# Kernel tuning notes

Hardware: AMD Instinct MI355X
Metric: run time of the kernel (lower is better)

## Reference

```python
import jax, jax.numpy as jnp
import numpy as np

B, L, D, C = 4, 512, 128, 128
EPS = 1e-7  # Keras backend epsilon


def setup_inputs() -> dict:
    key = jax.random.key(0)
    ks = jax.random.split(key, 4)
    inps = jax.random.normal(ks[0], (B, L, D), dtype=jnp.float32)
    # glorot_normal-ish scale for weights
    wei_t = jax.random.normal(ks[1], (D, C), dtype=jnp.float32) * (2.0 / (D + C)) ** 0.5
    wei_x = jax.random.normal(ks[2], (D, C), dtype=jnp.float32) * (2.0 / (D + C)) ** 0.5
    bxh = jnp.zeros((C,), dtype=jnp.float32)
    wei_a = jax.random.normal(ks[3], (C,), dtype=jnp.float32) * (2.0 / (C + 1)) ** 0.5
    bxa = jnp.zeros((), dtype=jnp.float32)
    return {"inps": inps, "wei_t": wei_t, "wei_x": wei_x, "bxh": bxh,
            "wei_a": wei_a, "bxa": bxa}


def reference(inps, wei_t, wei_x, bxh, wei_a, bxa):
    # Additive (Bahdanau-style) pairwise self-attention, no mask.
    qt = inps @ wei_t                      # [B, L, C] (query-side projection)
    kx = inps @ wei_x                      # [B, L, C] (key-side projection)
    # Pairwise hidden: [B, L, L, C]
    h = jnp.tanh(qt[:, :, None, :] + kx[:, None, :, :] + bxh)
    scores = jnp.einsum('bijc,c->bij', h, wei_a) + bxa  # [B, L, L]
    # activation_func=None -> linear (identity)
    e = jnp.exp(scores - jnp.max(scores, axis=-1, keepdims=True))
    a = e / (jnp.sum(e, axis=-1, keepdims=True) + EPS)   # [B, L, L]
    out = jnp.einsum('bij,bjd->bid', a, inps)            # [B, L, D]
    return out
```

## Files before the change

### kernel.cpp

```cpp
#include <hip/hip_runtime.h>

#define NB 4
#define SL 512
#define DD 128
#define CC 128

__device__ __forceinline__ float fexp2(float x) { return __builtin_amdgcn_exp2f(x); }
__device__ __forceinline__ float frcp(float x)  { return __builtin_amdgcn_rcpf(x); }

__global__ __launch_bounds__(256) void proj_kernel(
    const float* __restrict__ inps, const float* __restrict__ wei_t,
    const float* __restrict__ wei_x, const float* __restrict__ bxh,
    float* __restrict__ E, float* __restrict__ F)
{
    const float K2 = 2.8853900817779268f;
    const int row0 = blockIdx.x * 2;
    const int b    = row0 >> 9;
    const int i0   = row0 & 511;
    const int c    = threadIdx.x & 127;
    const int sel  = threadIdx.x >> 7;

    const float* W  = sel ? wei_x : wei_t;
    const float* r0 = inps + (size_t)row0 * DD;
    const float* r1 = r0 + DD;

    float a0 = 0.f, a1 = 0.f;
    #pragma unroll 8
    for (int k = 0; k < DD; ++k) {
        float w = W[k * CC + c];
        a0 = fmaf(r0[k], w, a0);
        a1 = fmaf(r1[k], w, a1);
    }

    if (sel == 0) {
        float bb = bxh[c];
        E[(size_t)(row0 + 0) * CC + c] = fexp2(K2 * (a0 + bb));
        E[(size_t)(row0 + 1) * CC + c] = fexp2(K2 * (a1 + bb));
    } else {
        float2 v = {fexp2(K2 * a0), fexp2(K2 * a1)};
        *reinterpret_cast<float2*>(&F[((size_t)b * CC + c) * SL + i0]) = v;
    }
}

__global__ __launch_bounds__(1024, 8) void attn_kernel(
    const float* __restrict__ inps, const float* __restrict__ wei_a,
    const float* __restrict__ E, const float* __restrict__ F,
    float* __restrict__ out)
{
    __shared__ float4 upk[CC];
    __shared__ float pool[4 * 16 * DD];
    __shared__ float scT[SL * 4];
    __shared__ float redw[4 * 4];

    const int blk = blockIdx.x;
    const int b   = blk >> 7;
    const int i0  = (blk & 127) * 4;
    const int bi0 = b * SL + i0;
    const int tid = threadIdx.x;
    const int jt  = tid & 255;
    const int cq  = tid >> 8;
    const int j0  = jt * 2;

    if (tid < CC) {
        float4 u;
        u.x = E[(size_t)(bi0 + 0) * CC + tid];
        u.y = E[(size_t)(bi0 + 1) * CC + tid];
        u.z = E[(size_t)(bi0 + 2) * CC + tid];
        u.w = E[(size_t)(bi0 + 3) * CC + tid];
        upk[tid] = u;
    }
    __syncthreads();

    const int c0 = cq * 32;
    const float* fb = F + ((size_t)b * CC + c0) * SL + j0;
    const float4* up = upk + c0;
    const float* wa = wei_a + c0;
    float sx[4] = {0.f, 0.f, 0.f, 0.f};
    float sy[4] = {0.f, 0.f, 0.f, 0.f};
    #pragma unroll 4
    for (int cp = 0; cp < 16; ++cp) {
        float2 f0 = *reinterpret_cast<const float2*>(&fb[(size_t)(2 * cp) * SL]);
        float2 f1 = *reinterpret_cast<const float2*>(&fb[(size_t)(2 * cp + 1) * SL]);
        float4 u0 = up[2 * cp];
        float4 u1 = up[2 * cp + 1];
        float wa0 = wa[2 * cp], wa1 = wa[2 * cp + 1];
        const float* u0p = reinterpret_cast<const float*>(&u0);
        const float* u1p = reinterpret_cast<const float*>(&u1);
        #pragma unroll
        for (int i = 0; i < 4; ++i) {
            float ax = fmaf(u0p[i], f0.x, 1.0f);
            float bx = fmaf(u1p[i], f1.x, 1.0f);
            float numx = fmaf(wa0, bx, wa1 * ax);
            sx[i] = fmaf(numx, frcp(ax * bx), sx[i]);
            float ay = fmaf(u0p[i], f0.y, 1.0f);
            float by = fmaf(u1p[i], f1.y, 1.0f);
            float numy = fmaf(wa0, by, wa1 * ay);
            sy[i] = fmaf(numy, frcp(ay * by), sy[i]);
        }
    }

    if (cq > 0) {
        float* m = &pool[(cq - 1) * 2304 + jt * 9];
        #pragma unroll
        for (int i = 0; i < 4; ++i) { m[i] = sx[i]; m[4 + i] = sy[i]; }
    }
    __syncthreads();

    if (cq == 0) {
        #pragma unroll
        for (int seg = 0; seg < 3; ++seg) {
            const float* m = &pool[seg * 2304 + jt * 9];
            #pragma unroll
            for (int i = 0; i < 4; ++i) { sx[i] += m[i]; sy[i] += m[4 + i]; }
        }
        const float KE = -2.8853900817779268f;
        float ex[4], ey[4];
        const int lane = tid & 63, wv = tid >> 6;
        #pragma unroll
        for (int i = 0; i < 4; ++i) {
            ex[i] = fexp2(sx[i] * KE);
            ey[i] = fexp2(sy[i] * KE);
            float t = ex[i] + ey[i];
            #pragma unroll
            for (int off = 32; off > 0; off >>= 1)
                t += __shfl_xor(t, off, 64);
            if (lane == 0) redw[i * 4 + wv] = t;
        }
        __syncthreads();
        float4 av0, av1;
        {
            float S0 = redw[0] + redw[1] + redw[2] + redw[3];
            float S1 = redw[4] + redw[5] + redw[6] + redw[7];
            float S2 = redw[8] + redw[9] + redw[10] + redw[11];
            float S3 = redw[12] + redw[13] + redw[14] + redw[15];
            float r0 = frcp(S0 + 1e-7f), r1 = frcp(S1 + 1e-7f);
            float r2 = frcp(S2 + 1e-7f), r3 = frcp(S3 + 1e-7f);
            av0 = make_float4(ex[0] * r0, ex[1] * r1, ex[2] * r2, ex[3] * r3);
            av1 = make_float4(ey[0] * r0, ey[1] * r1, ey[2] * r2, ey[3] * r3);
        }
        *reinterpret_cast<float4*>(&scT[j0 * 4])     = av0;
        *reinterpret_cast<float4*>(&scT[j0 * 4 + 4]) = av1;
    } else {
        __syncthreads();
    }
    __syncthreads();

    if (tid < 512) {
        const int dq = (tid & 31) * 4;
        const int jq = tid >> 5;
        const float* ibase = inps + (size_t)b * SL * DD;
        float4 acc0 = {0,0,0,0}, acc1 = {0,0,0,0}, acc2 = {0,0,0,0}, acc3 = {0,0,0,0};
        const int jb = jq * 32;
        #pragma unroll 4
        for (int jj = 0; jj < 32; ++jj) {
            int jx = jb + jj;
            float4 v  = *reinterpret_cast<const float4*>(ibase + (size_t)jx * DD + dq);
            float4 a4 = *reinterpret_cast<const float4*>(&scT[jx * 4]);
            acc0.x = fmaf(a4.x, v.x, acc0.x); acc0.y = fmaf(a4.x, v.y, acc0.y);
            acc0.z = fmaf(a4.x, v.z, acc0.z); acc0.w = fmaf(a4.x, v.w, acc0.w);
            acc1.x = fmaf(a4.y, v.x, acc1.x); acc1.y = fmaf(a4.y, v.y, acc1.y);
            acc1.z = fmaf(a4.y, v.z, acc1.z); acc1.w = fmaf(a4.y, v.w, acc1.w);
            acc2.x = fmaf(a4.z, v.x, acc2.x); acc2.y = fmaf(a4.z, v.y, acc2.y);
            acc2.z = fmaf(a4.z, v.z, acc2.z); acc2.w = fmaf(a4.z, v.w, acc2.w);
            acc3.x = fmaf(a4.w, v.x, acc3.x); acc3.y = fmaf(a4.w, v.y, acc3.y);
            acc3.z = fmaf(a4.w, v.z, acc3.z); acc3.w = fmaf(a4.w, v.w, acc3.w);
        }
        *reinterpret_cast<float4*>(&pool[(0 * 16 + jq) * DD + dq]) = acc0;
        *reinterpret_cast<float4*>(&pool[(1 * 16 + jq) * DD + dq]) = acc1;
        *reinterpret_cast<float4*>(&pool[(2 * 16 + jq) * DD + dq]) = acc2;
        *reinterpret_cast<float4*>(&pool[(3 * 16 + jq) * DD + dq]) = acc3;
    }
    __syncthreads();
    if (tid < 512) {
        int i = tid >> 7, d = tid & 127;
        float sum = 0.f;
        #pragma unroll
        for (int q = 0; q < 16; ++q) sum += pool[(i * 16 + q) * DD + d];
        out[(size_t)(bi0 + i) * DD + d] = sum;
    }
}

extern "C" void kernel_launch(void* const* d_in, const int* in_sizes, int n_in,
                              void* d_out, int out_size, void* d_ws, size_t ws_size,
                              hipStream_t stream) {
    const float* inps  = (const float*)d_in[0];
    const float* wei_t = (const float*)d_in[1];
    const float* wei_x = (const float*)d_in[2];
    const float* bxh   = (const float*)d_in[3];
    const float* wei_a = (const float*)d_in[4];
    float* out = (float*)d_out;

    float* E = (float*)d_ws;
    float* F = E + (size_t)NB * SL * CC;

    proj_kernel<<<NB * SL / 2, 256, 0, stream>>>(inps, wei_t, wei_x, bxh, E, F);
    attn_kernel<<<NB * SL / 4, 1024, 0, stream>>>(inps, wei_a, E, F, out);
}
```

Baseline: 90.21 us.

## Fuse query-side projection into attention kernel, keep only key projection separate

Moves the wei_t projection and its exp transform out of the projection kernel and into the attention kernel. Each attention block now computes its own four query rows' projections directly from inps instead of reading a precomputed E buffer. The projection kernel handles only the wei_x side with half as many blocks, which removes the E write/read round trip through global memory. In exchange, each attention block adds a serial 128-step dot product per thread before its main loop.

```diff
diff --git a/kernel.cpp b/kernel.cpp
--- a/kernel.cpp
+++ b/kernel.cpp
@@ -8,44 +8,35 @@
 __device__ __forceinline__ float fexp2(float x) { return __builtin_amdgcn_exp2f(x); }
 __device__ __forceinline__ float frcp(float x)  { return __builtin_amdgcn_rcpf(x); }
 
-__global__ __launch_bounds__(256) void proj_kernel(
-    const float* __restrict__ inps, const float* __restrict__ wei_t,
-    const float* __restrict__ wei_x, const float* __restrict__ bxh,
-    float* __restrict__ E, float* __restrict__ F)
+__global__ __launch_bounds__(256) void projF_kernel(
+    const float* __restrict__ inps, const float* __restrict__ wei_x,
+    float* __restrict__ F)
 {
     const float K2 = 2.8853900817779268f;
-    const int row0 = blockIdx.x * 2;
+    const int row0 = blockIdx.x * 4;
     const int b    = row0 >> 9;
     const int i0   = row0 & 511;
     const int c    = threadIdx.x & 127;
     const int sel  = threadIdx.x >> 7;
 
-    const float* W  = sel ? wei_x : wei_t;
-    const float* r0 = inps + (size_t)row0 * DD;
+    const float* r0 = inps + (size_t)(row0 + 2 * sel) * DD;
     const float* r1 = r0 + DD;
 
     float a0 = 0.f, a1 = 0.f;
     #pragma unroll 8
     for (int k = 0; k < DD; ++k) {
-        float w = W[k * CC + c];
+        float w = wei_x[k * CC + c];
         a0 = fmaf(r0[k], w, a0);
         a1 = fmaf(r1[k], w, a1);
     }
-
-    if (sel == 0) {
-        float bb = bxh[c];
-        E[(size_t)(row0 + 0) * CC + c] = fexp2(K2 * (a0 + bb));
-        E[(size_t)(row0 + 1) * CC + c] = fexp2(K2 * (a1 + bb));
-    } else {
-        float2 v = {fexp2(K2 * a0), fexp2(K2 * a1)};
-        *reinterpret_cast<float2*>(&F[((size_t)b * CC + c) * SL + i0]) = v;
-    }
+    float2 v = {fexp2(K2 * a0), fexp2(K2 * a1)};
+    *reinterpret_cast<float2*>(&F[((size_t)b * CC + c) * SL + i0 + 2 * sel]) = v;
 }
 
 __global__ __launch_bounds__(1024, 8) void attn_kernel(
     const float* __restrict__ inps, const float* __restrict__ wei_a,
-    const float* __restrict__ E, const float* __restrict__ F,
-    float* __restrict__ out)
+    const float* __restrict__ wei_t, const float* __restrict__ bxh,
+    const float* __restrict__ F, float* __restrict__ out)
 {
     __shared__ float4 upk[CC];
     __shared__ float pool[4 * 16 * DD];
@@ -61,13 +52,15 @@
     const int cq  = tid >> 8;
     const int j0  = jt * 2;
 
-    if (tid < CC) {
-        float4 u;
-        u.x = E[(size_t)(bi0 + 0) * CC + tid];
-        u.y = E[(size_t)(bi0 + 1) * CC + tid];
-        u.z = E[(size_t)(bi0 + 2) * CC + tid];
-        u.w = E[(size_t)(bi0 + 3) * CC + tid];
-        upk[tid] = u;
+    if (tid < 512) {
+        const int ii = tid >> 7, c = tid & 127;
+        const float K2 = 2.8853900817779268f;
+        const float* r = inps + (size_t)(bi0 + ii) * DD;
+        float acc = 0.f;
+        #pragma unroll 8
+        for (int k = 0; k < DD; ++k)
+            acc = fmaf(r[k], wei_t[k * CC + c], acc);
+        reinterpret_cast<float*>(&upk[c])[ii] = fexp2(K2 * (acc + bxh[c]));
     }
     __syncthreads();
 
@@ -190,9 +183,8 @@
     const float* wei_a = (const float*)d_in[4];
     float* out = (float*)d_out;
 
-    float* E = (float*)d_ws;
-    float* F = E + (size_t)NB * SL * CC;
+    float* F = (float*)d_ws;
 
-    proj_kernel<<<NB * SL / 2, 256, 0, stream>>>(inps, wei_t, wei_x, bxh, E, F);
-    attn_kernel<<<NB * SL / 4, 1024, 0, stream>>>(inps, wei_a, E, F, out);
+    projF_kernel<<<NB * SL / 4, 256, 0, stream>>>(inps, wei_x, F);
+    attn_kernel<<<NB * SL / 4, 1024, 0, stream>>>(inps, wei_a, wei_t, bxh, F, out);
 }
```

After: 97.35 us. 7.9% more time.
